# Performance work log

Hardware: AMD Instinct MI355X
Metric: run time of the kernel (lower is better)

## Reference

```python
import jax, jax.numpy as jnp
import numpy as np

NUM_NODES = 113      # nodes (ROIs) per graph, from __init__ default
NUM_GRAPHS = 4096    # graphs in the batch
IN_DIM, HID, EMB = 3, 128, 1024
GROUPS = 8
EPS = 1e-5


def _kaiming(key, fan_in, fan_out_dim, shape):
    # kaiming_normal_(mode='fan_out', nonlinearity='leaky_relu') with default a=sqrt(5)->gain irrelevant here;
    # torch uses gain = sqrt(2/(1+0.01^2)) for leaky_relu default slope; simple faithful-scale normal init.
    gain = jnp.sqrt(2.0 / (1.0 + 0.01 ** 2)).astype(jnp.float32)
    std = gain / jnp.sqrt(jnp.float32(fan_out_dim))
    return jax.random.normal(key, shape, dtype=jnp.float32) * std


def setup_inputs() -> dict:
    key = jax.random.key(0)
    ks = jax.random.split(key, 8)
    N = NUM_GRAPHS * NUM_NODES
    x = jax.random.normal(ks[0], (N, IN_DIM), dtype=jnp.float32)
    batch = jnp.repeat(jnp.arange(NUM_GRAPHS, dtype=jnp.int32), NUM_NODES)
    return {
        "x": x,
        "roi_scaler": jnp.ones((NUM_NODES, IN_DIM), dtype=jnp.float32),
        "W1": _kaiming(ks[1], IN_DIM, HID, (IN_DIM, HID)),
        "b1": jnp.zeros((HID,), jnp.float32),
        "gn_g": jnp.ones((HID,), jnp.float32),
        "gn_b": jnp.zeros((HID,), jnp.float32),
        "W2": _kaiming(ks[2], HID, HID, (HID, HID)),
        "b2": jnp.zeros((HID,), jnp.float32),
        "W3": _kaiming(ks[3], HID, 512, (HID, 512)),
        "b3": jnp.zeros((512,), jnp.float32),
        "bn_g": jnp.ones((512,), jnp.float32),
        "bn_b": jnp.zeros((512,), jnp.float32),
        "W4": _kaiming(ks[4], 512, EMB, (512, EMB)),
        "b4": jnp.zeros((EMB,), jnp.float32),
        "batch": batch,
    }


def _group_norm(h, gamma, beta):
    # torch GroupNorm on [N, C]: per-row, per-group normalization
    N, C = h.shape
    hg = h.reshape(N, GROUPS, C // GROUPS)
    mu = hg.mean(axis=-1, keepdims=True)
    var = hg.var(axis=-1, keepdims=True)
    hn = ((hg - mu) * jax.lax.rsqrt(var + EPS)).reshape(N, C)
    return hn * gamma + beta


def reference(x, roi_scaler, W1, b1, gn_g, gn_b, W2, b2, W3, b3, bn_g, bn_b, W4, b4, batch):
    # per-ROI learned scaling, tiled across graphs (node order is graph-major)
    h = x * jnp.tile(roi_scaler, (NUM_GRAPHS, 1))            # [N, 3]
    # node_net: Linear -> GroupNorm(8) -> LeakyReLU(0.2) -> Linear
    h = h @ W1 + b1                                          # [N, 128]
    h = _group_norm(h, gn_g, gn_b)
    h = jnp.where(h > 0, h, 0.2 * h)
    h = h @ W2 + b2                                          # [N, 128]
    # global_max_pool: segment max over graph id
    z = jax.ops.segment_max(h, batch, num_segments=NUM_GRAPHS)  # [G, 128]
    # projection: Linear -> BatchNorm1d (batch stats, no running stats) -> ReLU -> Linear
    p = z @ W3 + b3                                          # [G, 512]
    mu = p.mean(axis=0)
    var = p.var(axis=0)
    p = (p - mu) * jax.lax.rsqrt(var + EPS) * bn_g + bn_b
    p = jax.nn.relu(p)
    out = p @ W4 + b4                                        # [G, 1024]
    # F.normalize(p=2, dim=1)
    nrm = jnp.sqrt(jnp.sum(out * out, axis=1, keepdims=True))
    return out / jnp.maximum(nrm, 1e-12)
```

## Files before the change

### kernel.cpp

```cpp
#include <hip/hip_runtime.h>
#include <hip/hip_bf16.h>

typedef _Float16 f16_8 __attribute__((ext_vector_type(8)));
typedef _Float16 f16_4 __attribute__((ext_vector_type(4)));
typedef float f32x4 __attribute__((ext_vector_type(4)));

#define NNODES 113
#define NGRAPH 4096

#define Z_OFF    0u
#define PH_OFF   2097152u
#define PSUM_OFF 6291456u
#define PSQ_OFF  6815744u
#define PSN_OFF  7340032u
#define GC_OFF   10485760u
#define SA_OFF   10489856u
#define SD_OFF   10491904u
#define W2P_OFF  10493952u
#define W4P_OFF  10559488u

__global__ __launch_bounds__(256) void k0_prep(
    const float* __restrict__ W2, const float* __restrict__ W4,
    const float* __restrict__ W1, const float* __restrict__ b1,
    _Float16* __restrict__ w2p, _Float16* __restrict__ w4p,
    float* __restrict__ gc) {
  int b = blockIdx.x, t = threadIdx.x;
  if (b < 256) {
    __shared__ _Float16 T[32 * 72];
    int kt = b >> 4, nc = b & 15;
    int row = t >> 3, c8 = (t & 7) * 8;
    const float* src = &W4[(kt * 32 + row) * 1024 + nc * 64 + c8];
    float4 a0 = *(const float4*)src;
    float4 a1 = *(const float4*)(src + 4);
    f16_8 v = {(_Float16)a0.x, (_Float16)a0.y, (_Float16)a0.z, (_Float16)a0.w,
               (_Float16)a1.x, (_Float16)a1.y, (_Float16)a1.z, (_Float16)a1.w};
    *(f16_8*)&T[row * 72 + c8] = v;
    __syncthreads();
    int ntl = t >> 6, L = t & 63;
    f16_8 w;
#pragma unroll
    for (int j = 0; j < 8; j++)
      w[j] = T[((L >> 4) * 8 + j) * 72 + ntl * 16 + (L & 15)];
    *(f16_8*)&w4p[((kt * 64 + nc * 4 + ntl) * 64 + L) * 8] = w;
  } else if (b < 264) {
    int q0 = (b - 256) * 256 + t;
    int L = q0 & 63, nt = (q0 >> 6) & 7, kt = q0 >> 9;
    f16_8 v;
#pragma unroll
    for (int j = 0; j < 8; j++)
      v[j] = (_Float16)W2[(kt * 32 + ((L >> 4) << 3) + j) * 128 + (nt << 4) + (L & 15)];
    *(f16_8*)&w2p[((kt * 8 + nt) * 64 + L) * 8] = v;
  } else {
    if (t < 128) {
      float a0 = W1[t], a1 = W1[128 + t], a2 = W1[256 + t], bb = b1[t];
      float p[14] = {a0, a1, a2, bb,
                     a0 * a0, 2.f * a0 * a1, 2.f * a0 * a2,
                     a1 * a1, 2.f * a1 * a2, a2 * a2,
                     2.f * bb * a0, 2.f * bb * a1, 2.f * bb * a2, bb * bb};
#pragma unroll
      for (int m = 1; m < 16; m <<= 1)
#pragma unroll
        for (int k = 0; k < 14; k++) p[k] += __shfl_xor(p[k], m, 64);
      if ((t & 15) == 0) {
        int gg = t >> 4;
#pragma unroll
        for (int k = 0; k < 4; k++) gc[gg * 16 + k] = p[k] * 0.0625f;
#pragma unroll
        for (int k = 4; k < 14; k++) gc[gg * 16 + k] = p[k];
      }
    }
  }
}

__global__ __launch_bounds__(256, 4) void k1_nodenet(
    const float* __restrict__ x, const float* __restrict__ roi,
    const float* __restrict__ W1, const float* __restrict__ b1,
    const float* __restrict__ gn_g, const float* __restrict__ gn_b,
    const _Float16* __restrict__ w2p, const float* __restrict__ b2,
    const float* __restrict__ gc, float* __restrict__ z) {
  __shared__ float4 xs4[NNODES];
  __shared__ _Float16 A[128 * 136];
  int t = threadIdx.x, g = blockIdx.x;
  int lane = t & 63, wv = t >> 6, quad = lane >> 4, l16 = lane & 15;

  int o = t & 15;
  int gq = o >> 1;
  float gcv[14];
#pragma unroll
  for (int j = 0; j < 14; j++) gcv[j] = gc[gq * 16 + j];

  float pw0[8], pw1[8], pw2[8], pb[8], pg[8], pbe[8];
#pragma unroll
  for (int j = 0; j < 8; j++) {
    int c = o * 8 + j;
    pw0[j] = W1[c]; pw1[j] = W1[128 + c]; pw2[j] = W1[256 + c];
    pb[j] = b1[c];  pg[j] = gn_g[c];      pbe[j] = gn_b[c];
  }

  f16_8 bh[4][2];
#pragma unroll
  for (int kt = 0; kt < 4; kt++)
#pragma unroll
    for (int ni = 0; ni < 2; ni++)
      bh[kt][ni] = *(const f16_8*)&w2p[((kt * 8 + wv * 2 + ni) * 64 + lane) * 8];

  for (int i = t; i < NNODES * 3; i += 256) {
    float v = x[g * (NNODES * 3) + i] * roi[i];
    ((float*)xs4)[(i / 3) * 4 + (i % 3)] = v;
  }
  __syncthreads();

  for (int it = t; it < 2048; it += 256) {
    int n = it >> 4;
    f16_8 hv;
    if (n < NNODES) {
      float4 xv = xs4[n];
      float mu = fmaf(xv.z, gcv[2], fmaf(xv.y, gcv[1], fmaf(xv.x, gcv[0], gcv[3])));
      float qf = fmaf(xv.z, gcv[12], fmaf(xv.y, gcv[11], fmaf(xv.x, gcv[10], gcv[13])));
      float u0 = fmaf(xv.z, gcv[6], fmaf(xv.y, gcv[5], xv.x * gcv[4]));
      qf = fmaf(xv.x, u0, qf);
      float u1 = fmaf(xv.z, gcv[8], xv.y * gcv[7]);
      qf = fmaf(xv.y, u1, qf);
      qf = fmaf(xv.z * xv.z, gcv[9], qf);
      float var = fmaxf(qf * 0.0625f - mu * mu, 0.0f);
      float ia = rsqrtf(var + 1e-5f);
      float ib = -mu * ia;
#pragma unroll
      for (int j = 0; j < 8; j++) {
        float h = fmaf(xv.z, pw2[j], fmaf(xv.y, pw1[j], fmaf(xv.x, pw0[j], pb[j])));
        float y = fmaf(fmaf(h, ia, ib), pg[j], pbe[j]);
        y = (y > 0.0f) ? y : 0.2f * y;
        hv[j] = (_Float16)y;
      }
    } else {
#pragma unroll
      for (int j = 0; j < 8; j++) hv[j] = (_Float16)0.f;
    }
    *(f16_8*)&A[n * 136 + o * 8] = hv;
  }
  __syncthreads();

  f32x4 acc[2][8];
#pragma unroll
  for (int a = 0; a < 2; a++)
#pragma unroll
    for (int m = 0; m < 8; m++) acc[a][m] = (f32x4){0.f, 0.f, 0.f, 0.f};

#pragma unroll
  for (int kt = 0; kt < 4; kt++) {
    f16_8 ah[8];
#pragma unroll
    for (int mt = 0; mt < 8; mt++)
      ah[mt] = *(const f16_8*)&A[(mt * 16 + l16) * 136 + kt * 32 + quad * 8];
#pragma unroll
    for (int ni = 0; ni < 2; ni++)
#pragma unroll
      for (int mt = 0; mt < 8; mt++)
        acc[ni][mt] = __builtin_amdgcn_mfma_f32_16x16x32_f16(ah[mt], bh[kt][ni], acc[ni][mt], 0, 0, 0);
  }

#pragma unroll
  for (int ni = 0; ni < 2; ni++) {
    int nt = wv * 2 + ni;
    float m = -3.4e38f;
#pragma unroll
    for (int mt = 0; mt < 8; mt++)
#pragma unroll
      for (int r = 0; r < 4; r++) {
        int row = mt * 16 + quad * 4 + r;
        if (row < NNODES) m = fmaxf(m, acc[ni][mt][r]);
      }
    m = fmaxf(m, __shfl_xor(m, 16, 64));
    m = fmaxf(m, __shfl_xor(m, 32, 64));
    if (quad == 0) {
      int col = nt * 16 + l16;
      z[g * 128 + col] = m + b2[col];
    }
  }
}

__global__ __launch_bounds__(256) void k2_proj(
    const float* __restrict__ z, const float* __restrict__ W3,
    const float* __restrict__ b3, _Float16* __restrict__ ph,
    float* __restrict__ psum, float* __restrict__ psq) {
  __shared__ float zs[16 * 128];
  __shared__ float reds[8 * 128];
  __shared__ float redq[8 * 128];
  int t = threadIdx.x;
  int rb = blockIdx.x >> 2, cbb = blockIdx.x & 3;
  int gr0 = rb * 16, cc0 = cbb * 128;
  for (int i = t; i < 2048; i += 256) zs[i] = z[gr0 * 128 + i];
  int cg = t & 31, rg = t >> 5;
  int cc = cc0 + cg * 4;
  float4 bb = *(const float4*)&b3[cc];
  float a0[4] = {0.f, 0.f, 0.f, 0.f}, a1[4] = {0.f, 0.f, 0.f, 0.f};
  __syncthreads();

#pragma unroll 8
  for (int k = 0; k < 128; k++) {
    float4 w = *(const float4*)&W3[k * 512 + cc];
    float z0 = zs[rg * 256 + k];
    float z1 = zs[rg * 256 + 128 + k];
    a0[0] = fmaf(z0, w.x, a0[0]); a0[1] = fmaf(z0, w.y, a0[1]);
    a0[2] = fmaf(z0, w.z, a0[2]); a0[3] = fmaf(z0, w.w, a0[3]);
    a1[0] = fmaf(z1, w.x, a1[0]); a1[1] = fmaf(z1, w.y, a1[1]);
    a1[2] = fmaf(z1, w.z, a1[2]); a1[3] = fmaf(z1, w.w, a1[3]);
  }
  int r0 = gr0 + rg * 2;
  f16_4 h0, h1;
  float s[4], q[4];
#pragma unroll
  for (int j = 0; j < 4; j++) {
    float v0 = a0[j] + ((float*)&bb)[j];
    float v1 = a1[j] + ((float*)&bb)[j];
    h0[j] = (_Float16)v0; h1[j] = (_Float16)v1;
    s[j] = v0 + v1;
    q[j] = fmaf(v0, v0, v1 * v1);
  }
  *(f16_4*)&ph[r0 * 512 + cc] = h0;
  *(f16_4*)&ph[(r0 + 1) * 512 + cc] = h1;
#pragma unroll
  for (int j = 0; j < 4; j++) {
    reds[rg * 128 + cg * 4 + j] = s[j];
    redq[rg * 128 + cg * 4 + j] = q[j];
  }
  __syncthreads();
  if (t < 128) {
    float ss = 0.f, qq = 0.f;
#pragma unroll
    for (int r = 0; r < 8; r++) { ss += reds[r * 128 + t]; qq += redq[r * 128 + t]; }
    psum[rb * 512 + cc0 + t] = ss;
    psq[rb * 512 + cc0 + t] = qq;
  }
}

__global__ __launch_bounds__(512) void k3_stats(
    const float* __restrict__ psum, const float* __restrict__ psq,
    const float* __restrict__ bn_g, const float* __restrict__ bn_b,
    float* __restrict__ sa, float* __restrict__ sd) {
  int c = threadIdx.x;
  float s = 0.f, q = 0.f;
#pragma unroll 8
  for (int b = 0; b < 256; b++) {
    s += psum[b * 512 + c];
    q += psq[b * 512 + c];
  }
  float mu = s * (1.0f / 4096.0f);
  float var = fmaxf(q * (1.0f / 4096.0f) - mu * mu, 0.0f);
  float sc = bn_g[c] * rsqrtf(var + 1e-5f);
  sa[c] = sc;
  sd[c] = bn_b[c] - mu * sc;
}

__global__ __launch_bounds__(256) void k4a_gemm(
    const _Float16* __restrict__ ph, const float* __restrict__ sa,
    const float* __restrict__ sd, const _Float16* __restrict__ w4p,
    const float* __restrict__ b4, float* __restrict__ out,
    float* __restrict__ psn) {
  __shared__ _Float16 T[2][64 * 40];
  __shared__ float sas[512], sds[512];
  __shared__ float rred[4 * 64];
  int t = threadIdx.x;
  int rb = blockIdx.x & 63, cb = blockIdx.x >> 6;
  int lane = t & 63, wv = t >> 6, quad = lane >> 4, l16 = lane & 15;

  for (int i = t; i < 512; i += 256) { sas[i] = sa[i]; sds[i] = sd[i]; }

  int srow = t >> 2, seg8 = (t & 3) * 8;
  const _Float16* prow = &ph[(rb * 64 + srow) * 512];
  f16_8 pa = *(const f16_8*)&prow[seg8];
  f16_8 bfr[2];
#pragma unroll
  for (int ni = 0; ni < 2; ni++)
    bfr[ni] = *(const f16_8*)&w4p[((cb * 8 + wv * 2 + ni) * 64 + lane) * 8];
  __syncthreads();

  {
    f16_8 v;
#pragma unroll
    for (int j = 0; j < 8; j++) {
      float vv = fmaf((float)pa[j], sas[seg8 + j], sds[seg8 + j]);
      v[j] = (_Float16)fmaxf(vv, 0.0f);
    }
    *(f16_8*)&T[0][srow * 40 + seg8] = v;
  }
  __syncthreads();

  f32x4 acc[2][4];
#pragma unroll
  for (int a = 0; a < 2; a++)
#pragma unroll
    for (int m = 0; m < 4; m++) acc[a][m] = (f32x4){0.f, 0.f, 0.f, 0.f};

  for (int kt = 0; kt < 16; kt++) {
    int nb = kt + 1;
    f16_8 na;
    if (nb < 16) na = *(const f16_8*)&prow[nb * 32 + seg8];
    f16_8 bc0 = bfr[0], bc1 = bfr[1];
    if (nb < 16) {
#pragma unroll
      for (int ni = 0; ni < 2; ni++)
        bfr[ni] = *(const f16_8*)&w4p[((nb * 64 + cb * 8 + wv * 2 + ni) * 64 + lane) * 8];
    }
    const _Float16* Tb = &T[kt & 1][0];
#pragma unroll
    for (int mt = 0; mt < 4; mt++) {
      f16_8 af = *(const f16_8*)&Tb[(mt * 16 + l16) * 40 + quad * 8];
      acc[0][mt] = __builtin_amdgcn_mfma_f32_16x16x32_f16(af, bc0, acc[0][mt], 0, 0, 0);
      acc[1][mt] = __builtin_amdgcn_mfma_f32_16x16x32_f16(af, bc1, acc[1][mt], 0, 0, 0);
    }
    if (nb < 16) {
      int kc = nb * 32 + seg8;
      f16_8 v;
#pragma unroll
      for (int j = 0; j < 8; j++) {
        float vv = fmaf((float)na[j], sas[kc + j], sds[kc + j]);
        v[j] = (_Float16)fmaxf(vv, 0.0f);
      }
      *(f16_8*)&T[nb & 1][srow * 40 + seg8] = v;
    }
    __syncthreads();
  }

  float rsq[4][4];
#pragma unroll
  for (int mt = 0; mt < 4; mt++)
#pragma unroll
    for (int r = 0; r < 4; r++) rsq[mt][r] = 0.0f;
#pragma unroll
  for (int ni = 0; ni < 2; ni++) {
    int col = cb * 128 + (wv * 2 + ni) * 16 + l16;
    float bv = b4[col];
#pragma unroll
    for (int mt = 0; mt < 4; mt++)
#pragma unroll
      for (int r = 0; r < 4; r++) {
        float v = acc[ni][mt][r] + bv;
        out[(rb * 64 + mt * 16 + quad * 4 + r) * 1024 + col] = v;
        rsq[mt][r] = fmaf(v, v, rsq[mt][r]);
      }
  }
#pragma unroll
  for (int m = 1; m < 16; m <<= 1)
#pragma unroll
    for (int mt = 0; mt < 4; mt++)
#pragma unroll
      for (int r = 0; r < 4; r++) rsq[mt][r] += __shfl_xor(rsq[mt][r], m, 64);
  if (l16 == 0) {
#pragma unroll
    for (int mt = 0; mt < 4; mt++)
#pragma unroll
      for (int r = 0; r < 4; r++)
        rred[wv * 64 + mt * 16 + quad * 4 + r] = rsq[mt][r];
  }
  __syncthreads();
  if (t < 64) {
    float s = rred[t] + rred[64 + t] + rred[128 + t] + rred[192 + t];
    psn[cb * 4096 + rb * 64 + t] = s;
  }
}

__global__ __launch_bounds__(256) void k4b_norm(
    float* __restrict__ out, const float* __restrict__ psn) {
  int t = threadIdx.x;
  int row = blockIdx.x * 4 + (t >> 6);
  float s = 0.f;
#pragma unroll
  for (int cb = 0; cb < 8; cb++) s += psn[cb * 4096 + row];
  float inv = 1.0f / fmaxf(sqrtf(s), 1e-12f);
  int c0 = (t & 63) * 4;
#pragma unroll
  for (int it = 0; it < 4; it++) {
    float4 v = *(const float4*)&out[row * 1024 + it * 256 + c0];
    v.x *= inv; v.y *= inv; v.z *= inv; v.w *= inv;
    *(float4*)&out[row * 1024 + it * 256 + c0] = v;
  }
}

extern "C" void kernel_launch(void* const* d_in, const int* in_sizes, int n_in,
                              void* d_out, int out_size, void* d_ws, size_t ws_size,
                              hipStream_t stream) {
  const float* x   = (const float*)d_in[0];
  const float* roi = (const float*)d_in[1];
  const float* W1  = (const float*)d_in[2];
  const float* b1  = (const float*)d_in[3];
  const float* gng = (const float*)d_in[4];
  const float* gnb = (const float*)d_in[5];
  const float* W2  = (const float*)d_in[6];
  const float* b2  = (const float*)d_in[7];
  const float* W3  = (const float*)d_in[8];
  const float* b3  = (const float*)d_in[9];
  const float* bng = (const float*)d_in[10];
  const float* bnb = (const float*)d_in[11];
  const float* W4  = (const float*)d_in[12];
  const float* b4  = (const float*)d_in[13];
  float* out = (float*)d_out;

  char* ws = (char*)d_ws;
  float*    z    = (float*)(ws + Z_OFF);
  _Float16* ph   = (_Float16*)(ws + PH_OFF);
  float*    psum = (float*)(ws + PSUM_OFF);
  float*    psq  = (float*)(ws + PSQ_OFF);
  float*    psn  = (float*)(ws + PSN_OFF);
  float*    gc   = (float*)(ws + GC_OFF);
  float*    sa   = (float*)(ws + SA_OFF);
  float*    sd   = (float*)(ws + SD_OFF);
  _Float16* w2p  = (_Float16*)(ws + W2P_OFF);
  _Float16* w4p  = (_Float16*)(ws + W4P_OFF);

  k0_prep<<<265, 256, 0, stream>>>(W2, W4, W1, b1, w2p, w4p, gc);
  k1_nodenet<<<NGRAPH, 256, 0, stream>>>(x, roi, W1, b1, gng, gnb, w2p, b2, gc, z);
  k2_proj<<<1024, 256, 0, stream>>>(z, W3, b3, ph, psum, psq);
  k3_stats<<<1, 512, 0, stream>>>(psum, psq, bng, bnb, sa, sd);
  k4a_gemm<<<512, 256, 0, stream>>>(ph, sa, sd, w4p, b4, out, psn);
  k4b_norm<<<1024, 256, 0, stream>>>(out, psn);
}
```

Measured before the change: 175.4 us.

## Fuse L2 normalization into final GEMM and parallelize BN stats reduction

The final GEMM is restructured so each 512-thread block computes 16 full output rows across all 1024 columns. That lets the row L2 norm be computed in shared memory and applied before the single store, removing the separate normalize kernel and its extra read/write pass over the 16 MB output. The BN stats kernel is spread over 64 blocks with warp-shuffle reductions instead of running as one block. In exchange, W4 is re-read by every block, each block now holds only 16 rows (fewer rows of reuse per weight fetch), and register pressure rises from 16 B-fragments per thread.

```diff
diff --git a/kernel.cpp b/kernel.cpp
--- a/kernel.cpp
+++ b/kernel.cpp
@@ -12,7 +12,6 @@
 #define PH_OFF   2097152u
 #define PSUM_OFF 6291456u
 #define PSQ_OFF  6815744u
-#define PSN_OFF  7340032u
 #define GC_OFF   10485760u
 #define SA_OFF   10489856u
 #define SD_OFF   10491904u
@@ -234,146 +233,141 @@
   }
 }
 
-__global__ __launch_bounds__(512) void k3_stats(
+__global__ __launch_bounds__(256) void k3_stats(
     const float* __restrict__ psum, const float* __restrict__ psq,
     const float* __restrict__ bn_g, const float* __restrict__ bn_b,
     float* __restrict__ sa, float* __restrict__ sd) {
-  int c = threadIdx.x;
+  int t = threadIdx.x;
+  int c = blockIdx.x * 8 + (t >> 5);
+  int l = t & 31;
   float s = 0.f, q = 0.f;
-#pragma unroll 8
-  for (int b = 0; b < 256; b++) {
+#pragma unroll
+  for (int i = 0; i < 8; i++) {
+    int b = l + i * 32;
     s += psum[b * 512 + c];
     q += psq[b * 512 + c];
   }
-  float mu = s * (1.0f / 4096.0f);
-  float var = fmaxf(q * (1.0f / 4096.0f) - mu * mu, 0.0f);
-  float sc = bn_g[c] * rsqrtf(var + 1e-5f);
-  sa[c] = sc;
-  sd[c] = bn_b[c] - mu * sc;
-}
-
-__global__ __launch_bounds__(256) void k4a_gemm(
+#pragma unroll
+  for (int m = 1; m < 32; m <<= 1) {
+    s += __shfl_xor(s, m, 64);
+    q += __shfl_xor(q, m, 64);
+  }
+  if (l == 0) {
+    float mu = s * (1.0f / 4096.0f);
+    float var = fmaxf(q * (1.0f / 4096.0f) - mu * mu, 0.0f);
+    float sc = bn_g[c] * rsqrtf(var + 1e-5f);
+    sa[c] = sc;
+    sd[c] = bn_b[c] - mu * sc;
+  }
+}
+
+__global__ __launch_bounds__(512) void k4_gemm(
     const _Float16* __restrict__ ph, const float* __restrict__ sa,
     const float* __restrict__ sd, const _Float16* __restrict__ w4p,
-    const float* __restrict__ b4, float* __restrict__ out,
-    float* __restrict__ psn) {
-  __shared__ _Float16 T[2][64 * 40];
+    const float* __restrict__ b4, float* __restrict__ out) {
+  __shared__ _Float16 A[16 * 16 * 40];
   __shared__ float sas[512], sds[512];
-  __shared__ float rred[4 * 64];
+  __shared__ float rowsq[8][16];
+  __shared__ float rinv[16];
   int t = threadIdx.x;
-  int rb = blockIdx.x & 63, cb = blockIdx.x >> 6;
-  int lane = t & 63, wv = t >> 6, quad = lane >> 4, l16 = lane & 15;
-
-  for (int i = t; i < 512; i += 256) { sas[i] = sa[i]; sds[i] = sd[i]; }
-
-  int srow = t >> 2, seg8 = (t & 3) * 8;
-  const _Float16* prow = &ph[(rb * 64 + srow) * 512];
-  f16_8 pa = *(const f16_8*)&prow[seg8];
-  f16_8 bfr[2];
-#pragma unroll
-  for (int ni = 0; ni < 2; ni++)
-    bfr[ni] = *(const f16_8*)&w4p[((cb * 8 + wv * 2 + ni) * 64 + lane) * 8];
+  int rb = blockIdx.x;
+  int lane = t & 63, w = t >> 6, quad = lane >> 4, l16 = lane & 15;
+
+  sas[t] = sa[t];
+  sds[t] = sd[t];
+
+  const _Float16* p0 = &ph[(rb * 16 + w) * 512 + lane * 8];
+  const _Float16* p1 = &ph[(rb * 16 + w + 8) * 512 + lane * 8];
+  f16_8 pv0 = *(const f16_8*)p0;
+  f16_8 pv1 = *(const f16_8*)p1;
+  int nt0 = w * 8;
+  f16_8 bf0[8], bf1[8];
+#pragma unroll
+  for (int ni = 0; ni < 8; ni++)
+    bf0[ni] = *(const f16_8*)&w4p[((nt0 + ni) * 64 + lane) * 8];
   __syncthreads();
 
   {
-    f16_8 v;
-#pragma unroll
-    for (int j = 0; j < 8; j++) {
-      float vv = fmaf((float)pa[j], sas[seg8 + j], sds[seg8 + j]);
-      v[j] = (_Float16)fmaxf(vv, 0.0f);
-    }
-    *(f16_8*)&T[0][srow * 40 + seg8] = v;
-  }
-  __syncthreads();
-
-  f32x4 acc[2][4];
-#pragma unroll
-  for (int a = 0; a < 2; a++)
-#pragma unroll
-    for (int m = 0; m < 4; m++) acc[a][m] = (f32x4){0.f, 0.f, 0.f, 0.f};
-
-  for (int kt = 0; kt < 16; kt++) {
-    int nb = kt + 1;
-    f16_8 na;
-    if (nb < 16) na = *(const f16_8*)&prow[nb * 32 + seg8];
-    f16_8 bc0 = bfr[0], bc1 = bfr[1];
-    if (nb < 16) {
-#pragma unroll
-      for (int ni = 0; ni < 2; ni++)
-        bfr[ni] = *(const f16_8*)&w4p[((nb * 64 + cb * 8 + wv * 2 + ni) * 64 + lane) * 8];
-    }
-    const _Float16* Tb = &T[kt & 1][0];
-#pragma unroll
-    for (int mt = 0; mt < 4; mt++) {
-      f16_8 af = *(const f16_8*)&Tb[(mt * 16 + l16) * 40 + quad * 8];
-      acc[0][mt] = __builtin_amdgcn_mfma_f32_16x16x32_f16(af, bc0, acc[0][mt], 0, 0, 0);
-      acc[1][mt] = __builtin_amdgcn_mfma_f32_16x16x32_f16(af, bc1, acc[1][mt], 0, 0, 0);
-    }
-    if (nb < 16) {
-      int kc = nb * 32 + seg8;
-      f16_8 v;
-#pragma unroll
-      for (int j = 0; j < 8; j++) {
-        float vv = fmaf((float)na[j], sas[kc + j], sds[kc + j]);
-        v[j] = (_Float16)fmaxf(vv, 0.0f);
-      }
-      *(f16_8*)&T[nb & 1][srow * 40 + seg8] = v;
-    }
-    __syncthreads();
-  }
-
-  float rsq[4][4];
-#pragma unroll
-  for (int mt = 0; mt < 4; mt++)
-#pragma unroll
-    for (int r = 0; r < 4; r++) rsq[mt][r] = 0.0f;
-#pragma unroll
-  for (int ni = 0; ni < 2; ni++) {
-    int col = cb * 128 + (wv * 2 + ni) * 16 + l16;
-    float bv = b4[col];
-#pragma unroll
-    for (int mt = 0; mt < 4; mt++)
-#pragma unroll
-      for (int r = 0; r < 4; r++) {
-        float v = acc[ni][mt][r] + bv;
-        out[(rb * 64 + mt * 16 + quad * 4 + r) * 1024 + col] = v;
-        rsq[mt][r] = fmaf(v, v, rsq[mt][r]);
-      }
+    int kt_s = lane >> 2, c8 = lane & 3;
+    f32x4 s0 = *(const f32x4*)&sas[lane * 8];
+    f32x4 s1 = *(const f32x4*)&sas[lane * 8 + 4];
+    f32x4 d0 = *(const f32x4*)&sds[lane * 8];
+    f32x4 d1 = *(const f32x4*)&sds[lane * 8 + 4];
+    f16_8 o0, o1;
+#pragma unroll
+    for (int j = 0; j < 4; j++) {
+      float v = fmaf((float)pv0[j], s0[j], d0[j]);
+      o0[j] = (_Float16)fmaxf(v, 0.f);
+      v = fmaf((float)pv0[4 + j], s1[j], d1[j]);
+      o0[4 + j] = (_Float16)fmaxf(v, 0.f);
+      v = fmaf((float)pv1[j], s0[j], d0[j]);
+      o1[j] = (_Float16)fmaxf(v, 0.f);
+      v = fmaf((float)pv1[4 + j], s1[j], d1[j]);
+      o1[4 + j] = (_Float16)fmaxf(v, 0.f);
+    }
+    *(f16_8*)&A[(kt_s * 16 + w) * 40 + c8 * 8] = o0;
+    *(f16_8*)&A[(kt_s * 16 + w + 8) * 40 + c8 * 8] = o1;
+  }
+  __syncthreads();
+
+  f32x4 acc[8];
+#pragma unroll
+  for (int ni = 0; ni < 8; ni++) acc[ni] = (f32x4){0.f, 0.f, 0.f, 0.f};
+
+#pragma unroll
+  for (int kt2 = 0; kt2 < 8; kt2++) {
+    const int ktA = kt2 * 2, ktB = kt2 * 2 + 1;
+#pragma unroll
+    for (int ni = 0; ni < 8; ni++)
+      bf1[ni] = *(const f16_8*)&w4p[(((ktA + 1) * 64 + nt0 + ni) * 64 + lane) * 8];
+    f16_8 afA = *(const f16_8*)&A[(ktA * 16 + l16) * 40 + quad * 8];
+#pragma unroll
+    for (int ni = 0; ni < 8; ni++)
+      acc[ni] = __builtin_amdgcn_mfma_f32_16x16x32_f16(afA, bf0[ni], acc[ni], 0, 0, 0);
+    if (kt2 < 7) {
+#pragma unroll
+      for (int ni = 0; ni < 8; ni++)
+        bf0[ni] = *(const f16_8*)&w4p[(((ktB + 1) * 64 + nt0 + ni) * 64 + lane) * 8];
+    }
+    f16_8 afB = *(const f16_8*)&A[(ktB * 16 + l16) * 40 + quad * 8];
+#pragma unroll
+    for (int ni = 0; ni < 8; ni++)
+      acc[ni] = __builtin_amdgcn_mfma_f32_16x16x32_f16(afB, bf1[ni], acc[ni], 0, 0, 0);
+  }
+
+  float rsq[4] = {0.f, 0.f, 0.f, 0.f};
+#pragma unroll
+  for (int ni = 0; ni < 8; ni++) {
+    float bv = b4[w * 128 + ni * 16 + l16];
+#pragma unroll
+    for (int r = 0; r < 4; r++) {
+      float v = acc[ni][r] + bv;
+      acc[ni][r] = v;
+      rsq[r] = fmaf(v, v, rsq[r]);
+    }
   }
 #pragma unroll
   for (int m = 1; m < 16; m <<= 1)
 #pragma unroll
-    for (int mt = 0; mt < 4; mt++)
-#pragma unroll
-      for (int r = 0; r < 4; r++) rsq[mt][r] += __shfl_xor(rsq[mt][r], m, 64);
-  if (l16 == 0) {
-#pragma unroll
-    for (int mt = 0; mt < 4; mt++)
-#pragma unroll
-      for (int r = 0; r < 4; r++)
-        rred[wv * 64 + mt * 16 + quad * 4 + r] = rsq[mt][r];
-  }
-  __syncthreads();
-  if (t < 64) {
-    float s = rred[t] + rred[64 + t] + rred[128 + t] + rred[192 + t];
-    psn[cb * 4096 + rb * 64 + t] = s;
-  }
-}
-
-__global__ __launch_bounds__(256) void k4b_norm(
-    float* __restrict__ out, const float* __restrict__ psn) {
-  int t = threadIdx.x;
-  int row = blockIdx.x * 4 + (t >> 6);
-  float s = 0.f;
-#pragma unroll
-  for (int cb = 0; cb < 8; cb++) s += psn[cb * 4096 + row];
-  float inv = 1.0f / fmaxf(sqrtf(s), 1e-12f);
-  int c0 = (t & 63) * 4;
-#pragma unroll
-  for (int it = 0; it < 4; it++) {
-    float4 v = *(const float4*)&out[row * 1024 + it * 256 + c0];
-    v.x *= inv; v.y *= inv; v.z *= inv; v.w *= inv;
-    *(float4*)&out[row * 1024 + it * 256 + c0] = v;
+    for (int r = 0; r < 4; r++) rsq[r] += __shfl_xor(rsq[r], m, 64);
+  if (l16 == 0)
+#pragma unroll
+    for (int r = 0; r < 4; r++) rowsq[w][quad * 4 + r] = rsq[r];
+  __syncthreads();
+  if (t < 16) {
+    float s = 0.f;
+#pragma unroll
+    for (int ww = 0; ww < 8; ww++) s += rowsq[ww][t];
+    rinv[t] = 1.0f / fmaxf(sqrtf(s), 1e-12f);
+  }
+  __syncthreads();
+#pragma unroll
+  for (int r = 0; r < 4; r++) {
+    float inv = rinv[quad * 4 + r];
+    int obase = (rb * 16 + quad * 4 + r) * 1024 + w * 128 + l16;
+#pragma unroll
+    for (int ni = 0; ni < 8; ni++)
+      out[obase + ni * 16] = acc[ni][r] * inv;
   }
 }
 
@@ -401,7 +395,6 @@
   _Float16* ph   = (_Float16*)(ws + PH_OFF);
   float*    psum = (float*)(ws + PSUM_OFF);
   float*    psq  = (float*)(ws + PSQ_OFF);
-  float*    psn  = (float*)(ws + PSN_OFF);
   float*    gc   = (float*)(ws + GC_OFF);
   float*    sa   = (float*)(ws + SA_OFF);
   float*    sd   = (float*)(ws + SD_OFF);
@@ -411,7 +404,6 @@
   k0_prep<<<265, 256, 0, stream>>>(W2, W4, W1, b1, w2p, w4p, gc);
   k1_nodenet<<<NGRAPH, 256, 0, stream>>>(x, roi, W1, b1, gng, gnb, w2p, b2, gc, z);
   k2_proj<<<1024, 256, 0, stream>>>(z, W3, b3, ph, psum, psq);
-  k3_stats<<<1, 512, 0, stream>>>(psum, psq, bng, bnb, sa, sd);
-  k4a_gemm<<<512, 256, 0, stream>>>(ph, sa, sd, w4p, b4, out, psn);
-  k4b_norm<<<1024, 256, 0, stream>>>(out, psn);
-}
+  k3_stats<<<64, 256, 0, stream>>>(psum, psq, bng, bnb, sa, sd);
+  k4_gemm<<<256, 512, 0, stream>>>(ph, sa, sd, w4p, b4, out);
+}
```

New measurement: 164.3 us. 1.07x faster.
